# Kernel tuning notes

Hardware: AMD Instinct MI355X
Metric: run time of the kernel (lower is better)

Reference implementation:

```python
import jax, jax.numpy as jnp
import numpy as np

MAX_LORAS = 8
IN_SIZE = 4096
OUT_SIZE = 4096
B, S = 8, 1024


def setup_inputs() -> dict:
    key = jax.random.key(0)
    k1, k2, k3 = jax.random.split(key, 3)
    x = jax.random.normal(k1, (B, S, IN_SIZE), dtype=jnp.float32)
    adapter_ids = jax.random.randint(k2, (B,), 0, MAX_LORAS, dtype=jnp.int64)
    # memory_transpose=True layout: [max_loras, input_size, output_size]
    weight = jax.random.normal(k3, (MAX_LORAS, IN_SIZE, OUT_SIZE), dtype=jnp.float32) * 0.02
    return {"x": x, "adapter_ids": adapter_ids, "weight": weight}


def reference(x, adapter_ids, weight):
    # per-batch-row adapter weight gather: [B, in, out]
    w = weight[adapter_ids]
    # einsum 'bij,bjk->bik' (memory_transpose=True path)
    out = jnp.einsum('bsi,bio->bso', x, w)
    # reduce_from_tensor_model_parallel_region is identity on a single device
    return out
```

## Files before the change

### kernel.cpp

```cpp
#include <hip/hip_runtime.h>
#include <hip/hip_bf16.h>

typedef __attribute__((ext_vector_type(8))) short short8;
typedef __attribute__((ext_vector_type(4))) float f32x4;

constexpr int S_DIM   = 1024;
constexpr int IN_DIM  = 4096;
constexpr int OUT_DIM = 4096;
constexpr int NLORA   = 8;

typedef __attribute__((address_space(3))) unsigned char lds_byte_t;
typedef const __attribute__((address_space(1))) unsigned char glb_byte_t;

__device__ __forceinline__ unsigned short f2bf(float a) {
    union { __hip_bfloat16 h; unsigned short u; } c;
    c.h = __float2bfloat16(a);
    return c.u;
}
__device__ __forceinline__ unsigned int bf2pk(float a, float b) {
    return (unsigned int)f2bf(a) | ((unsigned int)f2bf(b) << 16);
}

__global__ __launch_bounds__(256)
void prep_w(const float* __restrict__ w, unsigned short* __restrict__ wt,
            const int* __restrict__ aids, int nb) {
    const int a = blockIdx.z;
    bool used = false;
    for (int i = 0; i < nb; ++i) used |= (aids[i] == a);
    if (!used) return;

    __shared__ __align__(16) unsigned short t[64][72];
    const int tid = threadIdx.x;
    const int n0 = blockIdx.x * 64;
    const int k0 = blockIdx.y * 64;
    const float* wb = w + (size_t)a * IN_DIM * OUT_DIM;

    const int nl = (tid & 15) * 4;
    #pragma unroll
    for (int p = 0; p < 4; ++p) {
        const int kl = p * 16 + (tid >> 4);
        f32x4 v = *reinterpret_cast<const f32x4*>(wb + (size_t)(k0 + kl) * OUT_DIM + n0 + nl);
        t[nl + 0][kl] = f2bf(v[0]);
        t[nl + 1][kl] = f2bf(v[1]);
        t[nl + 2][kl] = f2bf(v[2]);
        t[nl + 3][kl] = f2bf(v[3]);
    }
    __syncthreads();
    unsigned short* wtb = wt + (size_t)a * IN_DIM * OUT_DIM;
    const int chunk = tid & 7;
    #pragma unroll
    for (int q = 0; q < 2; ++q) {
        const int row = q * 32 + (tid >> 3);
        uint4 d = *reinterpret_cast<const uint4*>(&t[row][chunk * 8]);
        *reinterpret_cast<uint4*>(wtb + (size_t)(n0 + row) * IN_DIM + k0 + chunk * 8) = d;
    }
}

__global__ __launch_bounds__(256)
void prep_x(const float* __restrict__ x, unsigned short* __restrict__ xb, int n8) {
    const int stride = gridDim.x * blockDim.x;
    for (int i = blockIdx.x * blockDim.x + threadIdx.x; i < n8; i += stride) {
        const size_t o = (size_t)i * 8;
        f32x4 v0 = *reinterpret_cast<const f32x4*>(x + o);
        f32x4 v1 = *reinterpret_cast<const f32x4*>(x + o + 4);
        uint4 d;
        d.x = bf2pk(v0[0], v0[1]);
        d.y = bf2pk(v0[2], v0[3]);
        d.z = bf2pk(v1[0], v1[1]);
        d.w = bf2pk(v1[2], v1[3]);
        *reinterpret_cast<uint4*>(xb + o) = d;
    }
}

constexpr int BM = 256;
constexpr int BN = 256;
constexpr int BK = 64;
constexpr int NT = IN_DIM / BK;

__global__ __launch_bounds__(512, 2)
void gemm8p(const unsigned short* __restrict__ xb, const unsigned short* __restrict__ wt,
            const int* __restrict__ aids, float* __restrict__ out) {
    __shared__ __align__(16) unsigned char lds[2][65536];

    const int bid = blockIdx.x;
    const int swz = (bid & 7) * 64 + (bid >> 3);
    const int bz  = swz >> 6;
    const int rem = swz & 63;
    const int by  = rem >> 4;
    const int bx  = rem & 15;

    const int tid  = threadIdx.x;
    const int lane = tid & 63;
    const int wid  = tid >> 6;
    const int bm0  = by * BM;
    const int bn0  = bx * BN;
    const int aid  = aids[bz];

    const unsigned short* Ab = xb + ((size_t)bz * S_DIM + bm0) * IN_DIM;
    const unsigned short* Bb = wt + (size_t)aid * IN_DIM * OUT_DIM + (size_t)bn0 * IN_DIM;

    const int wr  = (wid >> 2) * 128;
    const int wc  = (wid & 3) * 64;
    const int l15 = lane & 15;
    const int lk  = lane >> 4;

    const int rl   = lane >> 3;
    const int ksrc = ((lane & 7) ^ rl) << 3;

    f32x4 acc[8][4] = {};

    auto stageA = [&](int buf, int k0, int h) {
        #pragma unroll
        for (int c = 0; c < 2; ++c) {
            const int chunk = h * 16 + wid * 2 + c;
            const int row   = chunk * 8 + rl;
            __builtin_amdgcn_global_load_lds(
                (glb_byte_t*)(Ab + (size_t)row * IN_DIM + k0 + ksrc),
                (lds_byte_t*)(&lds[buf][chunk * 1024]), 16, 0, 0);
        }
    };
    auto stageB = [&](int buf, int k0, int h) {
        #pragma unroll
        for (int c = 0; c < 2; ++c) {
            const int chunk = h * 16 + wid * 2 + c;
            const int row   = chunk * 8 + rl;
            __builtin_amdgcn_global_load_lds(
                (glb_byte_t*)(Bb + (size_t)row * IN_DIM + k0 + ksrc),
                (lds_byte_t*)(&lds[buf][32768 + chunk * 1024]), 16, 0, 0);
        }
    };

    auto readA = [&](int buf, int mh, short8 af[4][2]) {
        #pragma unroll
        for (int i = 0; i < 4; ++i) {
            const int row = wr + mh * 64 + i * 16 + l15;
            #pragma unroll
            for (int kc = 0; kc < 2; ++kc) {
                const int kb = kc * 64 + lk * 16;
                af[i][kc] = *reinterpret_cast<const short8*>(
                    &lds[buf][row * 128 + (kb ^ ((row & 7) << 4))]);
            }
        }
    };
    auto readB = [&](int buf, int np, short8 bf[2][2]) {
        #pragma unroll
        for (int nn = 0; nn < 2; ++nn) {
            const int row = wc + np * 32 + nn * 16 + l15;
            #pragma unroll
            for (int kc = 0; kc < 2; ++kc) {
                const int kb = kc * 64 + lk * 16;
                bf[nn][kc] = *reinterpret_cast<const short8*>(
                    &lds[buf][32768 + row * 128 + (kb ^ ((row & 7) << 4))]);
            }
        }
    };

    auto qmfma = [&](short8 af[4][2], short8 bf[2][2], int mh, int np) {
        __builtin_amdgcn_s_setprio(1);
        #pragma unroll
        for (int i = 0; i < 4; ++i)
            #pragma unroll
            for (int nn = 0; nn < 2; ++nn)
                #pragma unroll
                for (int kc = 0; kc < 2; ++kc)
                    acc[mh * 4 + i][np * 2 + nn] = __builtin_amdgcn_mfma_f32_16x16x32_bf16(
                        af[i][kc], bf[nn][kc], acc[mh * 4 + i][np * 2 + nn], 0, 0, 0);
        __builtin_amdgcn_s_setprio(0);
    };

    stageA(0, 0, 0); stageA(0, 0, 1); stageB(0, 0, 0); stageB(0, 0, 1);
    stageA(1, BK, 0); stageA(1, BK, 1); stageB(1, BK, 0); stageB(1, BK, 1);
    asm volatile("s_waitcnt vmcnt(8)" ::: "memory");
    __builtin_amdgcn_sched_barrier(0);
    __builtin_amdgcn_s_barrier();

    short8 a0[4][2], a1[4][2], b0[2][2], b1[2][2];

    #pragma unroll 1
    for (int j = 0; j < NT; ++j) {
        const int rb = j & 1;
        const int k2 = (j + 2) * BK;
        const bool pre = (j < NT - 2);

        readA(rb, 0, a0);
        readB(rb, 0, b0);
        __builtin_amdgcn_s_barrier();
        qmfma(a0, b0, 0, 0);
        __builtin_amdgcn_s_barrier();

        readB(rb, 1, b1);
        __builtin_amdgcn_s_barrier();
        qmfma(a0, b1, 0, 1);
        __builtin_amdgcn_s_barrier();
        __builtin_amdgcn_sched_barrier(0);

        readA(rb, 1, a1);
        if (pre) { stageB(rb, k2, 0); stageB(rb, k2, 1); }
        __builtin_amdgcn_s_barrier();
        qmfma(a1, b1, 1, 1);
        __builtin_amdgcn_s_barrier();
        __builtin_amdgcn_sched_barrier(0);

        if (pre) {
            stageA(rb, k2, 0); stageA(rb, k2, 1);
            asm volatile("s_waitcnt vmcnt(8)" ::: "memory");
        } else if (j == NT - 2) {
            asm volatile("s_waitcnt vmcnt(0)" ::: "memory");
        }
        __builtin_amdgcn_sched_barrier(0);
        __builtin_amdgcn_s_barrier();
        qmfma(a1, b0, 1, 0);
        __builtin_amdgcn_s_barrier();
    }

    float* obase = out + ((size_t)bz * S_DIM + bm0 + wr) * OUT_DIM + bn0 + wc;
    #pragma unroll
    for (int m = 0; m < 8; ++m) {
        #pragma unroll
        for (int n = 0; n < 4; ++n) {
            const int col = n * 16 + l15;
            #pragma unroll
            for (int r = 0; r < 4; ++r) {
                obase[(size_t)(m * 16 + lk * 4 + r) * OUT_DIM + col] = acc[m][n][r];
            }
        }
    }
}

constexpr int TMf = 128, TNf = 128, TKf = 64;
__global__ __launch_bounds__(256, 2)
void mlora_gemm(const float* __restrict__ x, const int* __restrict__ aids,
                const float* __restrict__ w, float* __restrict__ out) {
    __shared__ __align__(16) unsigned char As[TMf * TKf * 2];
    __shared__ __align__(16) unsigned char Bs[TNf * TKf * 2];

    const int tid  = threadIdx.x;
    const int lane = tid & 63;
    const int wid  = tid >> 6;
    const int bn0  = blockIdx.x * TNf;
    const int bm0  = blockIdx.y * TMf;
    const int bb   = blockIdx.z;
    const int aid  = aids[bb];

    const float* Abase = x + ((size_t)bb * S_DIM + bm0) * IN_DIM;
    const float* Bbase = w + (size_t)aid * IN_DIM * OUT_DIM + bn0;

    const int wr = (wid >> 1) * 64;
    const int wc = (wid & 1) * 64;

    f32x4 acc[4][4] = {};

    const int a_row4 = tid >> 4;
    const int a_k    = (tid & 15) * 4;
    const int b_n  = tid & 127;
    const int b_k0 = (tid >> 7) * 8;
    const int l15 = lane & 15;
    const int lk  = lane >> 4;

    for (int k0 = 0; k0 < IN_DIM; k0 += TKf) {
        #pragma unroll
        for (int p = 0; p < 8; ++p) {
            const int row = p * 16 + a_row4;
            f32x4 v = *reinterpret_cast<const f32x4*>(Abase + (size_t)row * IN_DIM + (k0 + a_k));
            uint2 d;
            d.x = bf2pk(v[0], v[1]);
            d.y = bf2pk(v[2], v[3]);
            const int off = row * (TKf * 2) + ((a_k * 2) ^ ((row & 7) << 4));
            *reinterpret_cast<uint2*>(&As[off]) = d;
        }
        {
            const float* bp = Bbase + (size_t)(k0 + b_k0) * OUT_DIM + b_n;
            #pragma unroll
            for (int g = 0; g < 4; ++g) {
                float f0 = bp[(size_t)(g * 16 + 0) * OUT_DIM];
                float f1 = bp[(size_t)(g * 16 + 1) * OUT_DIM];
                float f2 = bp[(size_t)(g * 16 + 2) * OUT_DIM];
                float f3 = bp[(size_t)(g * 16 + 3) * OUT_DIM];
                float f4 = bp[(size_t)(g * 16 + 4) * OUT_DIM];
                float f5 = bp[(size_t)(g * 16 + 5) * OUT_DIM];
                float f6 = bp[(size_t)(g * 16 + 6) * OUT_DIM];
                float f7 = bp[(size_t)(g * 16 + 7) * OUT_DIM];
                uint4 d;
                d.x = bf2pk(f0, f1);
                d.y = bf2pk(f2, f3);
                d.z = bf2pk(f4, f5);
                d.w = bf2pk(f6, f7);
                const int ks = b_k0 + g * 16;
                const int off = b_n * (TKf * 2) + ((ks * 2) ^ ((b_n & 7) << 4));
                *reinterpret_cast<uint4*>(&Bs[off]) = d;
            }
        }
        __syncthreads();
        #pragma unroll
        for (int kc = 0; kc < 2; ++kc) {
            const int kbyte = kc * 64 + lk * 16;
            short8 af[4], bfr[4];
            #pragma unroll
            for (int m = 0; m < 4; ++m) {
                const int row = wr + m * 16 + l15;
                af[m] = *reinterpret_cast<const short8*>(&As[row * (TKf * 2) + (kbyte ^ ((row & 7) << 4))]);
            }
            #pragma unroll
            for (int n = 0; n < 4; ++n) {
                const int row = wc + n * 16 + l15;
                bfr[n] = *reinterpret_cast<const short8*>(&Bs[row * (TKf * 2) + (kbyte ^ ((row & 7) << 4))]);
            }
            #pragma unroll
            for (int m = 0; m < 4; ++m) {
                #pragma unroll
                for (int n = 0; n < 4; ++n) {
                    acc[m][n] = __builtin_amdgcn_mfma_f32_16x16x32_bf16(af[m], bfr[n], acc[m][n], 0, 0, 0);
                }
            }
        }
        __syncthreads();
    }

    float* obase = out + ((size_t)bb * S_DIM + bm0 + wr) * OUT_DIM + bn0 + wc;
    #pragma unroll
    for (int m = 0; m < 4; ++m) {
        #pragma unroll
        for (int n = 0; n < 4; ++n) {
            const int col = n * 16 + l15;
            #pragma unroll
            for (int r = 0; r < 4; ++r) {
                obase[(size_t)(m * 16 + lk * 4 + r) * OUT_DIM + col] = acc[m][n][r];
            }
        }
    }
}

extern "C" void kernel_launch(void* const* d_in, const int* in_sizes, int n_in,
                              void* d_out, int out_size, void* d_ws, size_t ws_size,
                              hipStream_t stream) {
    const float* x    = (const float*)d_in[0];
    const int*   aids = (const int*)d_in[1];
    const float* w    = (const float*)d_in[2];
    float* out = (float*)d_out;
    const int nb = in_sizes[1];

    const size_t WT_BYTES = (size_t)NLORA * IN_DIM * OUT_DIM * 2;
    const size_t XB_BYTES = (size_t)nb * S_DIM * IN_DIM * 2;

    if (ws_size >= WT_BYTES + XB_BYTES) {
        unsigned short* wt = (unsigned short*)d_ws;
        unsigned short* xbuf = (unsigned short*)((char*)d_ws + WT_BYTES);

        dim3 gw(OUT_DIM / 64, IN_DIM / 64, NLORA);
        prep_w<<<gw, 256, 0, stream>>>(w, wt, aids, nb);

        const int n8 = nb * S_DIM * IN_DIM / 8;
        prep_x<<<4096, 256, 0, stream>>>(x, xbuf, n8);

        const int nwg = nb * (S_DIM / BM) * (OUT_DIM / BN);
        gemm8p<<<nwg, 512, 0, stream>>>(xbuf, wt, aids, out);
    } else {
        dim3 grid(OUT_DIM / TNf, S_DIM / TMf, nb);
        mlora_gemm<<<grid, 256, 0, stream>>>(x, aids, w, out);
    }
}
```

Before: 361.2 us.

## Drop weight prepass and load fp32 weights directly into registers in GEMM

Removes the separate kernel that transposed and converted the selected adapter weights to bf16, and instead has the main GEMM read fp32 weights directly from global memory into registers, converting them to bf16 before the MFMAs. Only the activation tile stays staged in LDS. This avoids a full read/write pass over the adapter weights but makes the B operand use strided scalar global loads, redundant loads across waves, and extra register and VALU pressure in the inner loop.

```diff
diff --git a/kernel.cpp b/kernel.cpp
--- a/kernel.cpp
+++ b/kernel.cpp
@@ -19,41 +19,6 @@
 }
 __device__ __forceinline__ unsigned int bf2pk(float a, float b) {
     return (unsigned int)f2bf(a) | ((unsigned int)f2bf(b) << 16);
-}
-
-__global__ __launch_bounds__(256)
-void prep_w(const float* __restrict__ w, unsigned short* __restrict__ wt,
-            const int* __restrict__ aids, int nb) {
-    const int a = blockIdx.z;
-    bool used = false;
-    for (int i = 0; i < nb; ++i) used |= (aids[i] == a);
-    if (!used) return;
-
-    __shared__ __align__(16) unsigned short t[64][72];
-    const int tid = threadIdx.x;
-    const int n0 = blockIdx.x * 64;
-    const int k0 = blockIdx.y * 64;
-    const float* wb = w + (size_t)a * IN_DIM * OUT_DIM;
-
-    const int nl = (tid & 15) * 4;
-    #pragma unroll
-    for (int p = 0; p < 4; ++p) {
-        const int kl = p * 16 + (tid >> 4);
-        f32x4 v = *reinterpret_cast<const f32x4*>(wb + (size_t)(k0 + kl) * OUT_DIM + n0 + nl);
-        t[nl + 0][kl] = f2bf(v[0]);
-        t[nl + 1][kl] = f2bf(v[1]);
-        t[nl + 2][kl] = f2bf(v[2]);
-        t[nl + 3][kl] = f2bf(v[3]);
-    }
-    __syncthreads();
-    unsigned short* wtb = wt + (size_t)a * IN_DIM * OUT_DIM;
-    const int chunk = tid & 7;
-    #pragma unroll
-    for (int q = 0; q < 2; ++q) {
-        const int row = q * 32 + (tid >> 3);
-        uint4 d = *reinterpret_cast<const uint4*>(&t[row][chunk * 8]);
-        *reinterpret_cast<uint4*>(wtb + (size_t)(n0 + row) * IN_DIM + k0 + chunk * 8) = d;
-    }
 }
 
 __global__ __launch_bounds__(256)
@@ -78,9 +43,9 @@
 constexpr int NT = IN_DIM / BK;
 
 __global__ __launch_bounds__(512, 2)
-void gemm8p(const unsigned short* __restrict__ xb, const unsigned short* __restrict__ wt,
+void gemm_f(const unsigned short* __restrict__ xb, const float* __restrict__ w,
             const int* __restrict__ aids, float* __restrict__ out) {
-    __shared__ __align__(16) unsigned char lds[2][65536];
+    __shared__ __align__(16) unsigned char As[2][32768];
 
     const int bid = blockIdx.x;
     const int swz = (bid & 7) * 64 + (bid >> 3);
@@ -97,7 +62,7 @@
     const int aid  = aids[bz];
 
     const unsigned short* Ab = xb + ((size_t)bz * S_DIM + bm0) * IN_DIM;
-    const unsigned short* Bb = wt + (size_t)aid * IN_DIM * OUT_DIM + (size_t)bn0 * IN_DIM;
+    const float* Wb = w + (size_t)aid * IN_DIM * OUT_DIM + bn0;
 
     const int wr  = (wid >> 2) * 128;
     const int wc  = (wid & 3) * 64;
@@ -116,46 +81,43 @@
             const int row   = chunk * 8 + rl;
             __builtin_amdgcn_global_load_lds(
                 (glb_byte_t*)(Ab + (size_t)row * IN_DIM + k0 + ksrc),
-                (lds_byte_t*)(&lds[buf][chunk * 1024]), 16, 0, 0);
-        }
-    };
-    auto stageB = [&](int buf, int k0, int h) {
-        #pragma unroll
-        for (int c = 0; c < 2; ++c) {
-            const int chunk = h * 16 + wid * 2 + c;
-            const int row   = chunk * 8 + rl;
-            __builtin_amdgcn_global_load_lds(
-                (glb_byte_t*)(Bb + (size_t)row * IN_DIM + k0 + ksrc),
-                (lds_byte_t*)(&lds[buf][32768 + chunk * 1024]), 16, 0, 0);
-        }
-    };
-
-    auto readA = [&](int buf, int mh, short8 af[4][2]) {
+                (lds_byte_t*)(&As[buf][chunk * 1024]), 16, 0, 0);
+        }
+    };
+    auto readA = [&](int buf, int mh, short8 (&a)[4][2]) {
         #pragma unroll
         for (int i = 0; i < 4; ++i) {
             const int row = wr + mh * 64 + i * 16 + l15;
             #pragma unroll
             for (int kc = 0; kc < 2; ++kc) {
                 const int kb = kc * 64 + lk * 16;
-                af[i][kc] = *reinterpret_cast<const short8*>(
-                    &lds[buf][row * 128 + (kb ^ ((row & 7) << 4))]);
-            }
-        }
-    };
-    auto readB = [&](int buf, int np, short8 bf[2][2]) {
-        #pragma unroll
-        for (int nn = 0; nn < 2; ++nn) {
-            const int row = wc + np * 32 + nn * 16 + l15;
+                a[i][kc] = *reinterpret_cast<const short8*>(
+                    &As[buf][row * 128 + (kb ^ ((row & 7) << 4))]);
+            }
+        }
+    };
+    auto issueB = [&](int np, int k0, float (&bf)[2][2][8]) {
+        const float* base = Wb + (size_t)k0 * OUT_DIM + wc + np * 32 + l15;
+        #pragma unroll
+        for (int nn = 0; nn < 2; ++nn)
+            #pragma unroll
+            for (int kc = 0; kc < 2; ++kc)
+                #pragma unroll
+                for (int kk = 0; kk < 8; ++kk)
+                    bf[nn][kc][kk] = base[(size_t)(kc * 32 + lk * 8 + kk) * OUT_DIM + nn * 16];
+    };
+    auto cvtB = [&](float (&bf)[2][2][8], short8 (&b)[2][2]) {
+        #pragma unroll
+        for (int nn = 0; nn < 2; ++nn)
             #pragma unroll
             for (int kc = 0; kc < 2; ++kc) {
-                const int kb = kc * 64 + lk * 16;
-                bf[nn][kc] = *reinterpret_cast<const short8*>(
-                    &lds[buf][32768 + row * 128 + (kb ^ ((row & 7) << 4))]);
-            }
-        }
-    };
-
-    auto qmfma = [&](short8 af[4][2], short8 bf[2][2], int mh, int np) {
+                short8 t;
+                #pragma unroll
+                for (int kk = 0; kk < 8; ++kk) t[kk] = (short)f2bf(bf[nn][kc][kk]);
+                b[nn][kc] = t;
+            }
+    };
+    auto qmfma = [&](short8 (&a)[4][2], short8 (&b)[2][2], int mh, int np) {
         __builtin_amdgcn_s_setprio(1);
         #pragma unroll
         for (int i = 0; i < 4; ++i)
@@ -164,51 +126,42 @@
                 #pragma unroll
                 for (int kc = 0; kc < 2; ++kc)
                     acc[mh * 4 + i][np * 2 + nn] = __builtin_amdgcn_mfma_f32_16x16x32_bf16(
-                        af[i][kc], bf[nn][kc], acc[mh * 4 + i][np * 2 + nn], 0, 0, 0);
+                        a[i][kc], b[nn][kc], acc[mh * 4 + i][np * 2 + nn], 0, 0, 0);
         __builtin_amdgcn_s_setprio(0);
     };
 
-    stageA(0, 0, 0); stageA(0, 0, 1); stageB(0, 0, 0); stageB(0, 0, 1);
-    stageA(1, BK, 0); stageA(1, BK, 1); stageB(1, BK, 0); stageB(1, BK, 1);
-    asm volatile("s_waitcnt vmcnt(8)" ::: "memory");
+    float b0f[2][2][8], b1f[2][2][8];
+    short8 b0[2][2], b1[2][2], a0[4][2], a1[4][2];
+
+    issueB(0, 0, b0f);
+    stageA(0, 0, 0); stageA(0, 0, 1);
+    stageA(1, BK, 0); stageA(1, BK, 1);
+    asm volatile("s_waitcnt vmcnt(4)" ::: "memory");
     __builtin_amdgcn_sched_barrier(0);
     __builtin_amdgcn_s_barrier();
-
-    short8 a0[4][2], a1[4][2], b0[2][2], b1[2][2];
 
     #pragma unroll 1
     for (int j = 0; j < NT; ++j) {
         const int rb = j & 1;
-        const int k2 = (j + 2) * BK;
-        const bool pre = (j < NT - 2);
 
         readA(rb, 0, a0);
-        readB(rb, 0, b0);
-        __builtin_amdgcn_s_barrier();
+        cvtB(b0f, b0);
+        __builtin_amdgcn_sched_barrier(0);
+        issueB(1, j * BK, b1f);
+        __builtin_amdgcn_sched_barrier(0);
         qmfma(a0, b0, 0, 0);
-        __builtin_amdgcn_s_barrier();
-
-        readB(rb, 1, b1);
-        __builtin_amdgcn_s_barrier();
+
+        cvtB(b1f, b1);
         qmfma(a0, b1, 0, 1);
-        __builtin_amdgcn_s_barrier();
-        __builtin_amdgcn_sched_barrier(0);
 
         readA(rb, 1, a1);
-        if (pre) { stageB(rb, k2, 0); stageB(rb, k2, 1); }
-        __builtin_amdgcn_s_barrier();
         qmfma(a1, b1, 1, 1);
-        __builtin_amdgcn_s_barrier();
-        __builtin_amdgcn_sched_barrier(0);
-
-        if (pre) {
-            stageA(rb, k2, 0); stageA(rb, k2, 1);
-            asm volatile("s_waitcnt vmcnt(8)" ::: "memory");
-        } else if (j == NT - 2) {
-            asm volatile("s_waitcnt vmcnt(0)" ::: "memory");
-        }
         __builtin_amdgcn_sched_barrier(0);
         __builtin_amdgcn_s_barrier();
+
+        if (j + 1 < NT) issueB(0, (j + 1) * BK, b0f);
+        if (j + 2 < NT) { stageA(rb, (j + 2) * BK, 0); stageA(rb, (j + 2) * BK, 1); }
+        __builtin_amdgcn_sched_barrier(0);
         qmfma(a1, b0, 1, 0);
         __builtin_amdgcn_s_barrier();
     }
@@ -231,8 +184,8 @@
 __global__ __launch_bounds__(256, 2)
 void mlora_gemm(const float* __restrict__ x, const int* __restrict__ aids,
                 const float* __restrict__ w, float* __restrict__ out) {
-    __shared__ __align__(16) unsigned char As[TMf * TKf * 2];
-    __shared__ __align__(16) unsigned char Bs[TNf * TKf * 2];
+    __shared__ __align__(16) unsigned char Asf[TMf * TKf * 2];
+    __shared__ __align__(16) unsigned char Bsf[TNf * TKf * 2];
 
     const int tid  = threadIdx.x;
     const int lane = tid & 63;
@@ -266,7 +219,7 @@
             d.x = bf2pk(v[0], v[1]);
             d.y = bf2pk(v[2], v[3]);
             const int off = row * (TKf * 2) + ((a_k * 2) ^ ((row & 7) << 4));
-            *reinterpret_cast<uint2*>(&As[off]) = d;
+            *reinterpret_cast<uint2*>(&Asf[off]) = d;
         }
         {
             const float* bp = Bbase + (size_t)(k0 + b_k0) * OUT_DIM + b_n;
@@ -287,7 +240,7 @@
                 d.w = bf2pk(f6, f7);
                 const int ks = b_k0 + g * 16;
                 const int off = b_n * (TKf * 2) + ((ks * 2) ^ ((b_n & 7) << 4));
-                *reinterpret_cast<uint4*>(&Bs[off]) = d;
+                *reinterpret_cast<uint4*>(&Bsf[off]) = d;
             }
         }
         __syncthreads();
@@ -298,12 +251,12 @@
             #pragma unroll
             for (int m = 0; m < 4; ++m) {
                 const int row = wr + m * 16 + l15;
-                af[m] = *reinterpret_cast<const short8*>(&As[row * (TKf * 2) + (kbyte ^ ((row & 7) << 4))]);
+                af[m] = *reinterpret_cast<const short8*>(&Asf[row * (TKf * 2) + (kbyte ^ ((row & 7) << 4))]);
             }
             #pragma unroll
             for (int n = 0; n < 4; ++n) {
                 const int row = wc + n * 16 + l15;
-                bfr[n] = *reinterpret_cast<const short8*>(&Bs[row * (TKf * 2) + (kbyte ^ ((row & 7) << 4))]);
+                bfr[n] = *reinterpret_cast<const short8*>(&Bsf[row * (TKf * 2) + (kbyte ^ ((row & 7) << 4))]);
             }
             #pragma unroll
             for (int m = 0; m < 4; ++m) {
@@ -339,21 +292,16 @@
     float* out = (float*)d_out;
     const int nb = in_sizes[1];
 
-    const size_t WT_BYTES = (size_t)NLORA * IN_DIM * OUT_DIM * 2;
     const size_t XB_BYTES = (size_t)nb * S_DIM * IN_DIM * 2;
 
-    if (ws_size >= WT_BYTES + XB_BYTES) {
-        unsigned short* wt = (unsigned short*)d_ws;
-        unsigned short* xbuf = (unsigned short*)((char*)d_ws + WT_BYTES);
-
-        dim3 gw(OUT_DIM / 64, IN_DIM / 64, NLORA);
-        prep_w<<<gw, 256, 0, stream>>>(w, wt, aids, nb);
+    if (ws_size >= XB_BYTES) {
+        unsigned short* xbuf = (unsigned short*)d_ws;
 
         const int n8 = nb * S_DIM * IN_DIM / 8;
         prep_x<<<4096, 256, 0, stream>>>(x, xbuf, n8);
 
         const int nwg = nb * (S_DIM / BM) * (OUT_DIM / BN);
-        gemm8p<<<nwg, 512, 0, stream>>>(xbuf, wt, aids, out);
+        gemm_f<<<nwg, 512, 0, stream>>>(xbuf, w, aids, out);
     } else {
         dim3 grid(OUT_DIM / TNf, S_DIM / TMf, nb);
         mlora_gemm<<<grid, 256, 0, stream>>>(x, aids, w, out);
```

New measurement: 786.2 us. 2.18x slower.
